# Optimization experiments

Measured on AMD Instinct MI355X. Metric: run time of the kernel, lower is better.

The kernel has to match this reference:

```python
import jax, jax.numpy as jnp
import numpy as np

T, B, DIM, N_STATE = 2048, 16, 1024, 1024
EPS = 1e-6


def setup_inputs() -> dict:
    key = jax.random.key(0)
    kx, kk, kv, kq = jax.random.split(key, 4)
    xavier = np.sqrt(2.0 / (N_STATE + DIM)).astype(np.float32)
    return {
        "x": jax.random.normal(kx, (T, B, DIM), dtype=jnp.float32),
        "W_k": jax.random.normal(kk, (N_STATE, DIM), dtype=jnp.float32) * xavier,
        "W_v": jax.random.normal(kv, (N_STATE, DIM), dtype=jnp.float32) * xavier,
        "W_q": jax.random.normal(kq, (N_STATE, DIM), dtype=jnp.float32) * xavier,
    }


def reference(x, W_k, W_v, W_q):
    # Projections for all timesteps at once: [T, B, n]
    k = jnp.einsum("tbd,nd->tbn", x, W_k)
    v = jnp.einsum("tbd,nd->tbn", x, W_v)
    q = jnp.einsum("tbd,nd->tbn", x, W_q)
    # L2-normalize k per (t, b) over the state dim (matches k_t.norm(dim=-1))
    k_norm = k / (jnp.linalg.norm(k, axis=-1, keepdims=True) + EPS)

    Tn, Bn, n = k.shape
    S0 = jnp.zeros((Bn, n), dtype=x.dtype)

    def step(S, inp):
        k_t, v_t, q_t = inp
        # Delta update with OUTPUT gating + tanh nonlinearity
        S_new = jnp.tanh(S * (1.0 - k_t * k_t) + v_t * k_t)
        Sq = S_new * q_t
        out = Sq * jax.nn.silu(Sq)
        return S_new, out

    S_final, output = jax.lax.scan(step, S0, (k_norm, v, q))
    return output, S_final
```

## Files before the change

### kernel.cpp

```cpp
#include <hip/hip_runtime.h>
#include <hip/hip_fp16.h>

#define T_STEPS 2048
#define BATCH 16
#define DIMD 1024
#define NSTATE 1024
#define MROWS (T_STEPS * BATCH)
#define NCH (BATCH * NSTATE)

typedef _Float16 f16x8 __attribute__((ext_vector_type(8)));
typedef float f32x4 __attribute__((ext_vector_type(4)));

#define GAS(p) ((const __attribute__((address_space(1))) void*)(p))
#define LAS(p) ((__attribute__((address_space(3))) void*)(p))

__global__ void cvt_kernel(const float* __restrict__ src, _Float16* __restrict__ dst, int n8) {
  int i = blockIdx.x * blockDim.x + threadIdx.x;
  if (i >= n8) return;
  const float4* s4 = (const float4*)src;
  float4 a = s4[(size_t)i * 2];
  float4 b = s4[(size_t)i * 2 + 1];
  f16x8 o;
  o[0] = (_Float16)a.x; o[1] = (_Float16)a.y; o[2] = (_Float16)a.z; o[3] = (_Float16)a.w;
  o[4] = (_Float16)b.x; o[5] = (_Float16)b.y; o[6] = (_Float16)b.z; o[7] = (_Float16)b.w;
  *((f16x8*)dst + i) = o;
}

__global__ void cvtW_kernel(const float* __restrict__ wk, const float* __restrict__ wv,
                            const float* __restrict__ wq, _Float16* __restrict__ dst) {
  const float* src = blockIdx.y == 0 ? wk : blockIdx.y == 1 ? wv : wq;
  int i = blockIdx.x * blockDim.x + threadIdx.x;
  const float4* s4 = (const float4*)src;
  float4 a = s4[(size_t)i * 2];
  float4 b = s4[(size_t)i * 2 + 1];
  f16x8 o;
  o[0] = (_Float16)a.x; o[1] = (_Float16)a.y; o[2] = (_Float16)a.z; o[3] = (_Float16)a.w;
  o[4] = (_Float16)b.x; o[5] = (_Float16)b.y; o[6] = (_Float16)b.z; o[7] = (_Float16)b.w;
  *((f16x8*)dst + (size_t)blockIdx.y * (NSTATE * DIMD / 8) + i) = o;
}

__global__ __launch_bounds__(512, 1) void gemm_kernel(const _Float16* __restrict__ A,
                                                      const _Float16* __restrict__ Wcat,
                                                      _Float16* __restrict__ KVQt,
                                                      float* __restrict__ rnpart) {
  __shared__ _Float16 lds[65536];
  const int tid = threadIdx.x;
  const int lane = tid & 63;
  const int w = tid >> 6;
  const int wm = w >> 2;
  const int wn = w & 3;

  const int bid = blockIdx.x;
  const int swz = (bid & 7) * 192 + (bid >> 3);
  const int mat = swz >> 9;
  const int rem = swz & 511;
  const int tileM = rem >> 2;
  const int tileN = rem & 3;

  const _Float16* Ag = A + (size_t)tileM * 256 * DIMD;
  const _Float16* Bg = Wcat + (size_t)mat * NSTATE * DIMD + (size_t)tileN * 256 * DIMD;

  const int s0 = tid, s1 = tid + 512;
  const int sr0 = s0 >> 2, sc0 = ((s0 & 3) ^ ((s0 >> 3) & 3)) * 8;
  const int sr1 = s1 >> 2, sc1 = ((s1 & 3) ^ ((s1 >> 3) & 3)) * 8;

#define STAGE_H(G, buf, reg, TT, h)                                                     \
  do {                                                                                  \
    __builtin_amdgcn_global_load_lds(                                                   \
        GAS(G + (size_t)sr0 * DIMD + (TT) * 64 + (h) * 32 + sc0),                       \
        LAS(lds + (buf) * 32768 + (reg) * 8192 + s0 * 8), 16, 0, 0);                    \
    __builtin_amdgcn_global_load_lds(                                                   \
        GAS(G + (size_t)sr1 * DIMD + (TT) * 64 + (h) * 32 + sc1),                       \
        LAS(lds + (buf) * 32768 + (reg) * 8192 + s1 * 8), 16, 0, 0);                    \
  } while (0)

  f32x4 acc[8][4];
#pragma unroll
  for (int m = 0; m < 8; ++m)
#pragma unroll
    for (int n = 0; n < 4; ++n)
      acc[m][n] = (f32x4){0.f, 0.f, 0.f, 0.f};

  const int fr = lane & 15;
  const int cbp = ((lane >> 4) ^ ((fr >> 1) & 3)) * 8;

  f16x8 aF[4], bF[4];

#define READS8(B, RA, RB)                                                               \
  do {                                                                                  \
    _Pragma("unroll") for (int m = 0; m < 4; ++m)                                       \
        aF[m] = *(const f16x8*)(lds + (B) * 32768 + (RA) * 8192 +                       \
                                (wm * 128 + m * 16 + fr) * 32 + cbp);                   \
    _Pragma("unroll") for (int n = 0; n < 4; ++n)                                       \
        bF[n] = *(const f16x8*)(lds + (B) * 32768 + (RB) * 8192 +                       \
                                (wn * 64 + n * 16 + fr) * 32 + cbp);                    \
  } while (0)

#define READS4(B, RA)                                                                   \
  do {                                                                                  \
    _Pragma("unroll") for (int m = 0; m < 4; ++m)                                       \
        aF[m] = *(const f16x8*)(lds + (B) * 32768 + (RA) * 8192 +                       \
                                (wm * 128 + (m + 4) * 16 + fr) * 32 + cbp);             \
  } while (0)

#define MFMA_LO                                                                         \
  _Pragma("unroll") for (int m = 0; m < 4; ++m)                                         \
  _Pragma("unroll") for (int n = 0; n < 4; ++n)                                         \
      acc[m][n] = __builtin_amdgcn_mfma_f32_16x16x32_f16(aF[m], bF[n], acc[m][n], 0, 0, 0)

#define MFMA_HI                                                                         \
  _Pragma("unroll") for (int m = 0; m < 4; ++m)                                         \
  _Pragma("unroll") for (int n = 0; n < 4; ++n)                                         \
      acc[m + 4][n] = __builtin_amdgcn_mfma_f32_16x16x32_f16(aF[m], bF[n], acc[m + 4][n], 0, 0, 0)

#define LGKM0_SB                                                                        \
  asm volatile("s_waitcnt lgkmcnt(0)" ::: "memory");                                    \
  __builtin_amdgcn_sched_barrier(0)

#define KT(T)                                                                           \
  do {                                                                                  \
    const int buf = (T) & 1, bufn = buf ^ 1;                                            \
                                \
    __builtin_amdgcn_s_barrier();                                                       \
    LGKM0_SB;                                                                           \
    __builtin_amdgcn_s_setprio(1); MFMA_LO; __builtin_amdgcn_s_setprio(0);              \
    __builtin_amdgcn_s_barrier();                                                       \
    READS4(buf, 0);                                                                     \
    if ((T) <= 14) STAGE_H(Bg, bufn, 2, (T) + 1, 0);                                    \
    __builtin_amdgcn_sched_barrier(0);                                                  \
                                                      \
    __builtin_amdgcn_s_barrier();                                                       \
    LGKM0_SB;                                                                           \
    __builtin_amdgcn_s_setprio(1); MFMA_HI; __builtin_amdgcn_s_setprio(0);              \
    if ((T) <= 14) { asm volatile("s_waitcnt vmcnt(4)" ::: "memory"); }                 \
    else           { asm volatile("s_waitcnt vmcnt(0)" ::: "memory"); }                 \
    __builtin_amdgcn_s_barrier();                        \
    __builtin_amdgcn_sched_barrier(0);                                                  \
    READS8(buf, 1, 3);                                                                  \
    if ((T) <= 14) STAGE_H(Ag, bufn, 1, (T) + 1, 1);                                    \
    __builtin_amdgcn_sched_barrier(0);                                                  \
                                                                \
    __builtin_amdgcn_s_barrier();                                                       \
    LGKM0_SB;                                                                           \
    __builtin_amdgcn_s_setprio(1); MFMA_LO; __builtin_amdgcn_s_setprio(0);              \
    __builtin_amdgcn_s_barrier();                                                       \
    READS4(buf, 1);                                                                     \
    if ((T) <= 14) STAGE_H(Bg, bufn, 3, (T) + 1, 1);                                    \
    __builtin_amdgcn_sched_barrier(0);                                                  \
                                                      \
    __builtin_amdgcn_s_barrier();                                                       \
    LGKM0_SB;                                                                           \
    __builtin_amdgcn_s_setprio(1); MFMA_HI; __builtin_amdgcn_s_setprio(0);              \
    if ((T) <= 14) {                                                                    \
      asm volatile("s_waitcnt vmcnt(4)" ::: "memory");                                  \
      __builtin_amdgcn_s_barrier();                  \
      __builtin_amdgcn_sched_barrier(0);                                                \
      READS8(bufn, 0, 2);                                                               \
      if ((T) <= 13) STAGE_H(Ag, buf, 0, (T) + 2, 0);                                   \
      __builtin_amdgcn_sched_barrier(0);                                                \
    }                                                                                   \
  } while (0)

  STAGE_H(Ag, 0, 0, 0, 0);
  STAGE_H(Bg, 0, 2, 0, 0);
  STAGE_H(Ag, 0, 1, 0, 1);
  STAGE_H(Bg, 0, 3, 0, 1);
  asm volatile("s_waitcnt vmcnt(4)" ::: "memory");
  __builtin_amdgcn_s_barrier();
  __builtin_amdgcn_sched_barrier(0);
  READS8(0, 0, 2);
  STAGE_H(Ag, 1, 0, 1, 0);
  __builtin_amdgcn_sched_barrier(0);

  KT(0);  KT(1);  KT(2);  KT(3);
  KT(4);  KT(5);  KT(6);  KT(7);
  KT(8);  KT(9);  KT(10); KT(11);
  KT(12); KT(13); KT(14); KT(15);

  const int cc = lane & 15;
  const int l4 = lane >> 4;
  _Float16* Cb = KVQt + (size_t)mat * ((size_t)MROWS * NSTATE) +
                 (size_t)(tileM * 2 + wm) * ((size_t)NCH * 8);
#pragma unroll
  for (int n = 0; n < 4; ++n)
#pragma unroll
    for (int j = 0; j < 4; ++j) {
      f16x8 pk;
#pragma unroll
      for (int m = 0; m < 8; ++m) pk[m] = (_Float16)acc[m][n][j];
      const int b = l4 * 4 + j;
      const int gcol = tileN * 256 + wn * 64 + n * 16 + cc;
      *(f16x8*)(Cb + ((size_t)(b * 1024 + gcol)) * 8) = pk;
    }

  if (mat == 0) {
#pragma unroll
    for (int m = 0; m < 8; ++m)
#pragma unroll
      for (int j = 0; j < 4; ++j) {
        float p = 0.f;
#pragma unroll
        for (int n = 0; n < 4; ++n) p += acc[m][n][j] * acc[m][n][j];
        p += __shfl_xor(p, 1);
        p += __shfl_xor(p, 2);
        p += __shfl_xor(p, 4);
        p += __shfl_xor(p, 8);
        if (cc == 0) {
          const int gr = tileM * 256 + wm * 128 + m * 16 + l4 * 4 + j;
          rnpart[(size_t)(tileN * 4 + wn) * MROWS + gr] = p;
        }
      }
  }
}

__global__ void rnfin_kernel(const float* __restrict__ part, float* __restrict__ rnT) {
  const int r = blockIdx.x * 256 + threadIdx.x;
  float s = 0.f;
#pragma unroll
  for (int i = 0; i < 16; ++i) s += part[(size_t)i * MROWS + r];
  rnT[(r & 15) * T_STEPS + (r >> 4)] = 1.f / (sqrtf(s) + 1e-6f);
}

#define STILE 16

#define LOADT(P, t0in)                                                        \
  do {                                                                        \
    const int tc = ((t0in) < T_STEPS) ? (t0in) : (T_STEPS - STILE);           \
    const size_t o0 = ((size_t)(tc >> 3) * NCH + c) * 8;                      \
    P##k0 = *(const f16x8*)(Kt + o0);                                         \
    P##k1 = *(const f16x8*)(Kt + o0 + (size_t)NCH * 8);                       \
    P##v0 = *(const f16x8*)(Vt + o0);                                         \
    P##v1 = *(const f16x8*)(Vt + o0 + (size_t)NCH * 8);                       \
    P##q0 = *(const f16x8*)(Qt + o0);                                         \
    P##q1 = *(const f16x8*)(Qt + o0 + (size_t)NCH * 8);                       \
    P##r0 = *(const f32x4*)(rnT + bb + tc);                                   \
    P##r1 = *(const f32x4*)(rnT + bb + tc + 4);                               \
    P##r2 = *(const f32x4*)(rnT + bb + tc + 8);                               \
    P##r3 = *(const f32x4*)(rnT + bb + tc + 12);                              \
  } while (0)

#define STEPT(P, t0)                                                          \
  do {                                                                        \
    float a2[STILE], b2[STILE], qf[STILE];                                    \
    _Pragma("unroll") for (int i = 0; i < STILE; ++i) {                       \
      float kf = (float)((i < 8) ? P##k0[i & 7] : P##k1[i & 7]);              \
      float vf = (float)((i < 8) ? P##v0[i & 7] : P##v1[i & 7]);              \
      float rv = (i < 4) ? P##r0[i & 3]                                       \
               : (i < 8) ? P##r1[i & 3]                                       \
               : (i < 12) ? P##r2[i & 3] : P##r3[i & 3];                      \
      float kn = kf * rv;                                                     \
      a2[i] = L2E2 - (L2E2 * kn) * kn;                                        \
      b2[i] = L2E2 * (vf * kn);                                               \
      qf[i] = (float)((i < 8) ? P##q0[i & 7] : P##q1[i & 7]);                 \
    }                                                                         \
    _Pragma("unroll") for (int i = 0; i < STILE; ++i) {                       \
      float u = fmaf(S, a2[i], b2[i]);                                        \
      float e = __builtin_amdgcn_exp2f(u);                                    \
      float r = __builtin_amdgcn_rcpf(e + 1.f);                               \
      S = fmaf(-2.f, r, 1.f);                                                 \
      float z = S * qf[i];                                                    \
      float sg = __builtin_amdgcn_rcpf(1.f + __builtin_amdgcn_exp2f(-L2E * z)); \
      out[(size_t)((t0) + i) * NCH + c] = z * z * sg;                         \
    }                                                                         \
  } while (0)

__global__ __launch_bounds__(64) void scan_kernel(const _Float16* __restrict__ Kt,
                                                  const _Float16* __restrict__ Vt,
                                                  const _Float16* __restrict__ Qt,
                                                  const float* __restrict__ rnT,
                                                  float* __restrict__ out,
                                                  float* __restrict__ sfin) {
  const int c = blockIdx.x * 64 + threadIdx.x;
  const int bb = (c >> 10) * T_STEPS;
  constexpr float L2E2 = 2.8853900817779268f;
  constexpr float L2E = 1.4426950408889634f;
  float S = 0.f;
  f16x8 Ak0, Ak1, Av0, Av1, Aq0, Aq1;
  f16x8 Bk0, Bk1, Bv0, Bv1, Bq0, Bq1;
  f16x8 Ck0, Ck1, Cv0, Cv1, Cq0, Cq1;
  f32x4 Ar0, Ar1, Ar2, Ar3, Br0, Br1, Br2, Br3, Cr0, Cr1, Cr2, Cr3;

  LOADT(A, 0);
  LOADT(B, STILE);
  for (int t0 = 0; t0 + 3 * STILE <= T_STEPS; t0 += 3 * STILE) {
    LOADT(C, t0 + 2 * STILE);
    STEPT(A, t0);
    LOADT(A, t0 + 3 * STILE);
    STEPT(B, t0 + STILE);
    LOADT(B, t0 + 4 * STILE);
    STEPT(C, t0 + 2 * STILE);
  }
  STEPT(A, T_STEPS - 2 * STILE);
  STEPT(B, T_STEPS - STILE);
  sfin[c] = S;
}

extern "C" void kernel_launch(void* const* d_in, const int* in_sizes, int n_in,
                              void* d_out, int out_size, void* d_ws, size_t ws_size,
                              hipStream_t stream) {
  const float* x = (const float*)d_in[0];
  const float* Wk = (const float*)d_in[1];
  const float* Wv = (const float*)d_in[2];
  const float* Wq = (const float*)d_in[3];

  char* ws = (char*)d_ws;
  _Float16* xh = (_Float16*)ws;
  _Float16* Wh = (_Float16*)(ws + 67108864ull);
  _Float16* KVQt = (_Float16*)(ws + 67108864ull + 6291456ull);
  float* rnpart = (float*)(ws + 67108864ull + 6291456ull + 201326592ull);
  float* rnT = (float*)(ws + 67108864ull + 6291456ull + 201326592ull + 2097152ull);

  int n8x = MROWS * DIMD / 8;
  cvt_kernel<<<(n8x + 255) / 256, 256, 0, stream>>>(x, xh, n8x);
  cvtW_kernel<<<dim3(NSTATE * DIMD / 8 / 256, 3), 256, 0, stream>>>(Wk, Wv, Wq, Wh);

  gemm_kernel<<<1536, 512, 0, stream>>>(xh, Wh, KVQt, rnpart);

  rnfin_kernel<<<MROWS / 256, 256, 0, stream>>>(rnpart, rnT);

  const _Float16* Kt = KVQt;
  const _Float16* Vt = KVQt + (size_t)MROWS * NSTATE;
  const _Float16* Qt = KVQt + 2ull * MROWS * NSTATE;
  float* outp = (float*)d_out;
  scan_kernel<<<NCH / 64, 64, 0, stream>>>(Kt, Vt, Qt, rnT, outp, outp + (size_t)MROWS * NSTATE);
}
```

Before: 382.9 us.

## Switch GEMM to 4 waves with 128x128 warp tiles and simpler double buffering

The GEMM block shrinks from 8 waves to 4, and each wave now computes a 128x128 output tile with 8x8 MFMA accumulators instead of 128x64. The finely interleaved half-stage pipeline with many barriers is replaced by a plain double-buffered loop: wait for all loads, barrier, prefetch the next K tile, then compute both K sub-slices. The aim is to raise MFMA work per LDS fragment read and cut barrier overhead. In exchange it doubles accumulator register use and leaves fewer waves to hide latency, and the full vmcnt(0) wait each iteration may expose load latency. The norm partials and their reduction are updated to match the new wave layout.

Result: slower. 421.5 us (+10.1%).

```diff
diff --git a/kernel.cpp b/kernel.cpp
--- a/kernel.cpp
+++ b/kernel.cpp
@@ -39,7 +39,7 @@
   *((f16x8*)dst + (size_t)blockIdx.y * (NSTATE * DIMD / 8) + i) = o;
 }
 
-__global__ __launch_bounds__(512, 1) void gemm_kernel(const _Float16* __restrict__ A,
+__global__ __launch_bounds__(256, 1) void gemm_kernel(const _Float16* __restrict__ A,
                                                       const _Float16* __restrict__ Wcat,
                                                       _Float16* __restrict__ KVQt,
                                                       float* __restrict__ rnpart) {
@@ -47,8 +47,8 @@
   const int tid = threadIdx.x;
   const int lane = tid & 63;
   const int w = tid >> 6;
-  const int wm = w >> 2;
-  const int wn = w & 3;
+  const int wm = w >> 1;
+  const int wn = w & 1;
 
   const int bid = blockIdx.x;
   const int swz = (bid & 7) * 192 + (bid >> 3);
@@ -60,118 +60,62 @@
   const _Float16* Ag = A + (size_t)tileM * 256 * DIMD;
   const _Float16* Bg = Wcat + (size_t)mat * NSTATE * DIMD + (size_t)tileN * 256 * DIMD;
 
-  const int s0 = tid, s1 = tid + 512;
-  const int sr0 = s0 >> 2, sc0 = ((s0 & 3) ^ ((s0 >> 3) & 3)) * 8;
-  const int sr1 = s1 >> 2, sc1 = ((s1 & 3) ^ ((s1 >> 3) & 3)) * 8;
-
-#define STAGE_H(G, buf, reg, TT, h)                                                     \
-  do {                                                                                  \
-    __builtin_amdgcn_global_load_lds(                                                   \
-        GAS(G + (size_t)sr0 * DIMD + (TT) * 64 + (h) * 32 + sc0),                       \
-        LAS(lds + (buf) * 32768 + (reg) * 8192 + s0 * 8), 16, 0, 0);                    \
-    __builtin_amdgcn_global_load_lds(                                                   \
-        GAS(G + (size_t)sr1 * DIMD + (TT) * 64 + (h) * 32 + sc1),                       \
-        LAS(lds + (buf) * 32768 + (reg) * 8192 + s1 * 8), 16, 0, 0);                    \
-  } while (0)
-
-  f32x4 acc[8][4];
+#define STAGE_REG(G, buf, reg, koff)                                                    \
+  do {                                                                                  \
+    _Pragma("unroll") for (int i = 0; i < 4; ++i) {                                     \
+      const int s = i * 256 + tid;                                                      \
+      const int sr = s >> 2, sc = ((s & 3) ^ ((s >> 3) & 3)) * 8;                       \
+      __builtin_amdgcn_global_load_lds(GAS(G + (size_t)sr * DIMD + (koff) + sc),        \
+                                       LAS(lds + (buf) * 32768 + (reg) * 8192 + s * 8), \
+                                       16, 0, 0);                                       \
+    }                                                                                   \
+  } while (0)
+
+#define STAGE_TILE(buf, TT)                                                             \
+  do {                                                                                  \
+    STAGE_REG(Ag, buf, 0, (TT) * 64);                                                   \
+    STAGE_REG(Bg, buf, 2, (TT) * 64);                                                   \
+    STAGE_REG(Ag, buf, 1, (TT) * 64 + 32);                                              \
+    STAGE_REG(Bg, buf, 3, (TT) * 64 + 32);                                              \
+  } while (0)
+
+  f32x4 acc[8][8];
 #pragma unroll
   for (int m = 0; m < 8; ++m)
 #pragma unroll
-    for (int n = 0; n < 4; ++n)
+    for (int n = 0; n < 8; ++n)
       acc[m][n] = (f32x4){0.f, 0.f, 0.f, 0.f};
 
   const int fr = lane & 15;
   const int cbp = ((lane >> 4) ^ ((fr >> 1) & 3)) * 8;
 
-  f16x8 aF[4], bF[4];
-
-#define READS8(B, RA, RB)                                                               \
-  do {                                                                                  \
-    _Pragma("unroll") for (int m = 0; m < 4; ++m)                                       \
-        aF[m] = *(const f16x8*)(lds + (B) * 32768 + (RA) * 8192 +                       \
+#define COMPUTE_KS(buf, ks)                                                             \
+  do {                                                                                  \
+    f16x8 aF[8], bF[8];                                                                 \
+    _Pragma("unroll") for (int m = 0; m < 8; ++m)                                       \
+        aF[m] = *(const f16x8*)(lds + (buf) * 32768 + (ks) * 8192 +                     \
                                 (wm * 128 + m * 16 + fr) * 32 + cbp);                   \
-    _Pragma("unroll") for (int n = 0; n < 4; ++n)                                       \
-        bF[n] = *(const f16x8*)(lds + (B) * 32768 + (RB) * 8192 +                       \
-                                (wn * 64 + n * 16 + fr) * 32 + cbp);                    \
-  } while (0)
-
-#define READS4(B, RA)                                                                   \
-  do {                                                                                  \
-    _Pragma("unroll") for (int m = 0; m < 4; ++m)                                       \
-        aF[m] = *(const f16x8*)(lds + (B) * 32768 + (RA) * 8192 +                       \
-                                (wm * 128 + (m + 4) * 16 + fr) * 32 + cbp);             \
-  } while (0)
-
-#define MFMA_LO                                                                         \
-  _Pragma("unroll") for (int m = 0; m < 4; ++m)                                         \
-  _Pragma("unroll") for (int n = 0; n < 4; ++n)                                         \
-      acc[m][n] = __builtin_amdgcn_mfma_f32_16x16x32_f16(aF[m], bF[n], acc[m][n], 0, 0, 0)
-
-#define MFMA_HI                                                                         \
-  _Pragma("unroll") for (int m = 0; m < 4; ++m)                                         \
-  _Pragma("unroll") for (int n = 0; n < 4; ++n)                                         \
-      acc[m + 4][n] = __builtin_amdgcn_mfma_f32_16x16x32_f16(aF[m], bF[n], acc[m + 4][n], 0, 0, 0)
-
-#define LGKM0_SB                                                                        \
-  asm volatile("s_waitcnt lgkmcnt(0)" ::: "memory");                                    \
-  __builtin_amdgcn_sched_barrier(0)
+    _Pragma("unroll") for (int n = 0; n < 8; ++n)                                       \
+        bF[n] = *(const f16x8*)(lds + (buf) * 32768 + (2 + (ks)) * 8192 +               \
+                                (wn * 128 + n * 16 + fr) * 32 + cbp);                   \
+    _Pragma("unroll") for (int m = 0; m < 8; ++m)                                       \
+    _Pragma("unroll") for (int n = 0; n < 8; ++n)                                       \
+        acc[m][n] = __builtin_amdgcn_mfma_f32_16x16x32_f16(aF[m], bF[n], acc[m][n], 0, 0, 0); \
+  } while (0)
 
 #define KT(T)                                                                           \
   do {                                                                                  \
-    const int buf = (T) & 1, bufn = buf ^ 1;                                            \
-                                \
+    const int buf = (T) & 1;                                                            \
+    asm volatile("s_waitcnt vmcnt(0)" ::: "memory");                                    \
     __builtin_amdgcn_s_barrier();                                                       \
-    LGKM0_SB;                                                                           \
-    __builtin_amdgcn_s_setprio(1); MFMA_LO; __builtin_amdgcn_s_setprio(0);              \
-    __builtin_amdgcn_s_barrier();                                                       \
-    READS4(buf, 0);                                                                     \
-    if ((T) <= 14) STAGE_H(Bg, bufn, 2, (T) + 1, 0);                                    \
     __builtin_amdgcn_sched_barrier(0);                                                  \
-                                                      \
-    __builtin_amdgcn_s_barrier();                                                       \
-    LGKM0_SB;                                                                           \
-    __builtin_amdgcn_s_setprio(1); MFMA_HI; __builtin_amdgcn_s_setprio(0);              \
-    if ((T) <= 14) { asm volatile("s_waitcnt vmcnt(4)" ::: "memory"); }                 \
-    else           { asm volatile("s_waitcnt vmcnt(0)" ::: "memory"); }                 \
-    __builtin_amdgcn_s_barrier();                        \
+    if ((T) < 15) STAGE_TILE(buf ^ 1, (T) + 1);                                         \
     __builtin_amdgcn_sched_barrier(0);                                                  \
-    READS8(buf, 1, 3);                                                                  \
-    if ((T) <= 14) STAGE_H(Ag, bufn, 1, (T) + 1, 1);                                    \
-    __builtin_amdgcn_sched_barrier(0);                                                  \
-                                                                \
-    __builtin_amdgcn_s_barrier();                                                       \
-    LGKM0_SB;                                                                           \
-    __builtin_amdgcn_s_setprio(1); MFMA_LO; __builtin_amdgcn_s_setprio(0);              \
-    __builtin_amdgcn_s_barrier();                                                       \
-    READS4(buf, 1);                                                                     \
-    if ((T) <= 14) STAGE_H(Bg, bufn, 3, (T) + 1, 1);                                    \
-    __builtin_amdgcn_sched_barrier(0);                                                  \
-                                                      \
-    __builtin_amdgcn_s_barrier();                                                       \
-    LGKM0_SB;                                                                           \
-    __builtin_amdgcn_s_setprio(1); MFMA_HI; __builtin_amdgcn_s_setprio(0);              \
-    if ((T) <= 14) {                                                                    \
-      asm volatile("s_waitcnt vmcnt(4)" ::: "memory");                                  \
-      __builtin_amdgcn_s_barrier();                  \
-      __builtin_amdgcn_sched_barrier(0);                                                \
-      READS8(bufn, 0, 2);                                                               \
-      if ((T) <= 13) STAGE_H(Ag, buf, 0, (T) + 2, 0);                                   \
-      __builtin_amdgcn_sched_barrier(0);                                                \
-    }                                                                                   \
-  } while (0)
-
-  STAGE_H(Ag, 0, 0, 0, 0);
-  STAGE_H(Bg, 0, 2, 0, 0);
-  STAGE_H(Ag, 0, 1, 0, 1);
-  STAGE_H(Bg, 0, 3, 0, 1);
-  asm volatile("s_waitcnt vmcnt(4)" ::: "memory");
-  __builtin_amdgcn_s_barrier();
-  __builtin_amdgcn_sched_barrier(0);
-  READS8(0, 0, 2);
-  STAGE_H(Ag, 1, 0, 1, 0);
-  __builtin_amdgcn_sched_barrier(0);
-
+    COMPUTE_KS(buf, 0);                                                                 \
+    COMPUTE_KS(buf, 1);                                                                 \
+  } while (0)
+
+  STAGE_TILE(0, 0);
   KT(0);  KT(1);  KT(2);  KT(3);
   KT(4);  KT(5);  KT(6);  KT(7);
   KT(8);  KT(9);  KT(10); KT(11);
@@ -182,14 +126,14 @@
   _Float16* Cb = KVQt + (size_t)mat * ((size_t)MROWS * NSTATE) +
                  (size_t)(tileM * 2 + wm) * ((size_t)NCH * 8);
 #pragma unroll
-  for (int n = 0; n < 4; ++n)
+  for (int n = 0; n < 8; ++n)
 #pragma unroll
     for (int j = 0; j < 4; ++j) {
       f16x8 pk;
 #pragma unroll
       for (int m = 0; m < 8; ++m) pk[m] = (_Float16)acc[m][n][j];
       const int b = l4 * 4 + j;
-      const int gcol = tileN * 256 + wn * 64 + n * 16 + cc;
+      const int gcol = tileN * 256 + wn * 128 + n * 16 + cc;
       *(f16x8*)(Cb + ((size_t)(b * 1024 + gcol)) * 8) = pk;
     }
 
@@ -200,14 +144,14 @@
       for (int j = 0; j < 4; ++j) {
         float p = 0.f;
 #pragma unroll
-        for (int n = 0; n < 4; ++n) p += acc[m][n][j] * acc[m][n][j];
+        for (int n = 0; n < 8; ++n) p += acc[m][n][j] * acc[m][n][j];
         p += __shfl_xor(p, 1);
         p += __shfl_xor(p, 2);
         p += __shfl_xor(p, 4);
         p += __shfl_xor(p, 8);
         if (cc == 0) {
           const int gr = tileM * 256 + wm * 128 + m * 16 + l4 * 4 + j;
-          rnpart[(size_t)(tileN * 4 + wn) * MROWS + gr] = p;
+          rnpart[(size_t)(tileN * 2 + wn) * MROWS + gr] = p;
         }
       }
   }
@@ -217,7 +161,7 @@
   const int r = blockIdx.x * 256 + threadIdx.x;
   float s = 0.f;
 #pragma unroll
-  for (int i = 0; i < 16; ++i) s += part[(size_t)i * MROWS + r];
+  for (int i = 0; i < 8; ++i) s += part[(size_t)i * MROWS + r];
   rnT[(r & 15) * T_STEPS + (r >> 4)] = 1.f / (sqrtf(s) + 1e-6f);
 }
 
@@ -314,7 +258,7 @@
   cvt_kernel<<<(n8x + 255) / 256, 256, 0, stream>>>(x, xh, n8x);
   cvtW_kernel<<<dim3(NSTATE * DIMD / 8 / 256, 3), 256, 0, stream>>>(Wk, Wv, Wq, Wh);
 
-  gemm_kernel<<<1536, 512, 0, stream>>>(xh, Wh, KVQt, rnpart);
+  gemm_kernel<<<1536, 256, 0, stream>>>(xh, Wh, KVQt, rnpart);
 
   rnfin_kernel<<<MROWS / 256, 256, 0, stream>>>(rnpart, rnT);
 
```
